# Kernel optimization log

Hardware: AMD Instinct MI355X
Metric: run time of the kernel (lower is better)

The kernel has to match this reference:

```python
import jax, jax.numpy as jnp
import numpy as np

NUM_SCENES = 7
SHAPE = [512, 512, 256, 64]  # layer dims: 512->512->256->64
BATCH = 16384


def _xavier(key, shape):
    # nn.init.xavier_normal_ on (s, in, out): fan_in/fan_out from last two dims
    fan_in, fan_out = shape[-2], shape[-1]
    std = np.sqrt(2.0 / (fan_in + fan_out)).astype(np.float32)
    return jax.random.normal(key, shape, dtype=jnp.float32) * std


def setup_inputs() -> dict:
    key = jax.random.key(0)
    ks = jax.random.split(key, 16)
    inp = {
        "x": jax.random.normal(ks[0], (BATCH, SHAPE[0]), dtype=jnp.float32),
        "scene": jax.random.randint(ks[1], (BATCH,), 1, NUM_SCENES + 1, dtype=jnp.int64),
    }
    for i in range(3):
        din, dout = SHAPE[i], SHAPE[i + 1]
        inp[f"W{i}"] = _xavier(ks[2 + 4 * i], (NUM_SCENES, din, dout))
        inp[f"b{i}"] = jnp.zeros((NUM_SCENES, dout), dtype=jnp.float32)
        inp[f"gW{i}"] = _xavier(ks[3 + 4 * i], (1, din, dout))
        inp[f"gb{i}"] = jnp.zeros((1, dout), dtype=jnp.float32)
    return inp


def _star_linear(x, scene0, W, b, gW, gb, relu):
    # W: (S, in, out), gW: (1, in, out). Equivalent to gathering W[scene0]
    # and doing x[:,None,:] @ (w * gW), but computed as a dense GEMM over
    # all scenes followed by a per-sample select (avoids B*in*out gather).
    scaled = W * gW                                   # (S, in, out)
    out_all = jnp.einsum('bi,sio->bso', x, scaled)    # (B, S, out)
    out = jnp.take_along_axis(out_all, scene0[:, None, None], axis=1)[:, 0, :]
    out = out + b[scene0] + gb[0]
    if relu:
        out = jnp.maximum(out, 0.0)
    return out  # dropout is identity at eval


def reference(x, scene, W0, b0, gW0, gb0, W1, b1, gW1, gb1, W2, b2, gW2, gb2):
    scene0 = (scene - 1).astype(jnp.int32)
    h = _star_linear(x, scene0, W0, b0, gW0, gb0, relu=True)
    h = _star_linear(h, scene0, W1, b1, gW1, gb1, relu=True)
    h = _star_linear(h, scene0, W2, b2, gW2, gb2, relu=False)  # drop=True -> no relu
    return h
```

## Files before the change

kernel.cpp:

```cpp
#include <hip/hip_runtime.h>
#include <hip/hip_bf16.h>
#include <stdint.h>


#define BATCH   16384
#define NSCENE  7
#define TM      128
#define NBLK    (BATCH / 256)
#define MT_MAX  (BATCH / TM + NSCENE)
#define PADMAX  (BATCH + NSCENE * TM)

typedef __bf16 bf16x8 __attribute__((ext_vector_type(8)));
typedef float  f32x4  __attribute__((ext_vector_type(4)));

__device__ __forceinline__ ushort f2bf(float f) {
  union { float f; uint32_t u; } v; v.f = f;
  uint32_t r = (v.u + 0x7FFFu + ((v.u >> 16) & 1u)) >> 16;
  return (ushort)r;
}
__device__ __forceinline__ uint32_t pk2(float a, float b) {
  union { __hip_bfloat162 h; uint32_t u; } cv;
  cv.h = __float22bfloat162_rn(make_float2(a, b));
  return cv.u;
}
__device__ __forceinline__ void async16(const void* g, void* lds) {
  __builtin_amdgcn_global_load_lds(
      (const __attribute__((address_space(1))) uint32_t*)g,
      (__attribute__((address_space(3))) uint32_t*)lds, 16, 0, 0);
}

__device__ __forceinline__ void st_tile(const float* __restrict__ W,
                                        const float* __restrict__ gW,
                                        ushort* __restrict__ sT,
                                        int K, int N, int s, int n0, int k0,
                                        int tid) {
  __shared__ float tl[32][33];
  int tx = tid & 31, ty = tid >> 5;
  const float* Wp = W + (size_t)s * K * N;
#pragma unroll
  for (int i = 0; i < 4; i++) {
    int k = k0 + ty + i * 8;
    tl[ty + i * 8][tx] = Wp[(size_t)k * N + n0 + tx] * gW[(size_t)k * N + n0 + tx];
  }
  __syncthreads();
#pragma unroll
  for (int i = 0; i < 4; i++) {
    int n = n0 + ty + i * 8;
    sT[((size_t)s * N + n) * K + k0 + tx] = f2bf(tl[tx][ty + i * 8]);
  }
}

#define NB_W0 (16 * 16 * 7)
#define NB_W1 (8 * 16 * 7)
#define NB_W2 (2 * 8 * 7)
#define NB_BIAS 23
#define NB_CNT NBLK

__global__ __launch_bounds__(256) void prep_k(
    const float* __restrict__ W0, const float* __restrict__ gW0,
    const float* __restrict__ W1, const float* __restrict__ gW1,
    const float* __restrict__ W2, const float* __restrict__ gW2,
    const float* __restrict__ b0, const float* __restrict__ gb0,
    const float* __restrict__ b1, const float* __restrict__ gb1,
    const float* __restrict__ b2, const float* __restrict__ gb2,
    const int* __restrict__ scene,
    ushort* __restrict__ sT0, ushort* __restrict__ sT1, ushort* __restrict__ sT2,
    float* __restrict__ bias0, float* __restrict__ bias1, float* __restrict__ bias2,
    int* __restrict__ bcnt, int* __restrict__ rank) {
  int bid = blockIdx.x, tid = threadIdx.x;
  if (bid < NB_W0) {
    int l = bid;
    st_tile(W0, gW0, sT0, 512, 512, l / 256, (l % 16) * 32, ((l / 16) % 16) * 32, tid);
  } else if (bid < NB_W0 + NB_W1) {
    int l = bid - NB_W0;
    st_tile(W1, gW1, sT1, 512, 256, l / 128, (l % 8) * 32, ((l / 8) % 16) * 32, tid);
  } else if (bid < NB_W0 + NB_W1 + NB_W2) {
    int l = bid - NB_W0 - NB_W1;
    st_tile(W2, gW2, sT2, 256, 64, l / 16, (l % 2) * 32, ((l / 2) % 8) * 32, tid);
  } else if (bid < NB_W0 + NB_W1 + NB_W2 + NB_BIAS) {
    int t = (bid - NB_W0 - NB_W1 - NB_W2) * 256 + tid;
    if (t < 7 * 512) bias0[t] = b0[t] + gb0[t & 511];
    else if (t < 7 * 512 + 7 * 256) { int i = t - 7 * 512; bias1[i] = b1[i] + gb1[i & 255]; }
    else if (t < 7 * 512 + 7 * 256 + 7 * 64) { int i = t - 7 * 512 - 7 * 256; bias2[i] = b2[i] + gb2[i & 63]; }
  } else {
    __shared__ int l[NSCENE];
    if (tid < NSCENE) l[tid] = 0;
    __syncthreads();
    int blk = bid - NB_W0 - NB_W1 - NB_W2 - NB_BIAS;
    int i = blk * 256 + tid;
    int pos = atomicAdd(&l[scene[i] - 1], 1);
    rank[i] = pos;
    __syncthreads();
    if (tid < NSCENE) bcnt[blk * NSCENE + tid] = l[tid];
  }
}

__global__ void plan_k(const int* __restrict__ bcnt, int* __restrict__ meta,
                       int* __restrict__ bbase, int* __restrict__ idxp) {
  __shared__ int tot[NSCENE], pstart[NSCENE], pend[NSCENE];
  int tid = threadIdx.x;
  if (tid < NSCENE) {
    int c = 0;
    for (int b = 0; b < NBLK; b++) c += bcnt[b * NSCENE + tid];
    tot[tid] = c;
  }
  __syncthreads();
  if (tid == 0) {
    int po = 0, t = 0;
    for (int s = 0; s < NSCENE; s++) {
      meta[16 + s] = po;
      int tiles = (tot[s] + TM - 1) / TM;
      pstart[s] = po + tot[s];
      pend[s] = po + tiles * TM;
      for (int j = 0; j < tiles; j++) { meta[32 + t] = s; meta[192 + t] = po + j * TM; t++; }
      po += tiles * TM;
    }
    meta[24] = t;
  }
  __syncthreads();
  if (tid < NSCENE) {
    int run = meta[16 + tid];
    for (int b = 0; b < NBLK; b++) { bbase[b * NSCENE + tid] = run; run += bcnt[b * NSCENE + tid]; }
  }
  for (int s = 0; s < NSCENE; s++)
    for (int i = pstart[s] + tid; i < pend[s]; i += 256) idxp[i] = -1;
}

__global__ __launch_bounds__(256) void xc_k(const float* __restrict__ x,
                                            const int* __restrict__ scene,
                                            const int* __restrict__ rank,
                                            const int* __restrict__ bbase,
                                            int* __restrict__ idxp,
                                            ushort* __restrict__ xc) {
  int r = blockIdx.x * 8 + (threadIdx.x >> 5);
  int s = scene[r] - 1;
  int d = bbase[(r >> 8) * NSCENE + s] + rank[r];
  if ((threadIdx.x & 31) == 0) idxp[d] = r;
  int c = (threadIdx.x & 31) * 16;
  const float4* p = (const float4*)(x + (size_t)r * 512 + c);
  float4 f0 = p[0], f1 = p[1], f2 = p[2], f3 = p[3];
  uint4 v0, v1;
  v0.x = pk2(f0.x, f0.y); v0.y = pk2(f0.z, f0.w);
  v0.z = pk2(f1.x, f1.y); v0.w = pk2(f1.z, f1.w);
  v1.x = pk2(f2.x, f2.y); v1.y = pk2(f2.z, f2.w);
  v1.z = pk2(f3.x, f3.y); v1.w = pk2(f3.z, f3.w);
  uint4* q = (uint4*)(xc + (size_t)d * 512 + c);
  q[0] = v0; q[1] = v1;
}

__global__ __launch_bounds__(256) void gemm0_k(
    const ushort* __restrict__ ain, const ushort* __restrict__ bw,
    const float* __restrict__ bias, const int* __restrict__ meta,
    ushort* __restrict__ hout) {
  int j = blockIdx.x;
  int t = j >> 1;
  if (t >= meta[24]) return;
  int sc = meta[32 + t];
  int mrow0 = meta[192 + t] + (j & 1) * 64;
  int nb = blockIdx.y;

  __shared__ __align__(16) ushort Abuf[64 * 64];
  __shared__ __align__(16) ushort Bbuf[128 * 64];

  int tid = threadIdx.x;
  int lane = tid & 63, wid = tid >> 6;

  f32x4 acc[4][2];
#pragma unroll
  for (int mt = 0; mt < 4; mt++)
#pragma unroll
    for (int nt = 0; nt < 2; nt++) acc[mt][nt] = (f32x4){0.f, 0.f, 0.f, 0.f};

  const ushort* bwS = bw + ((size_t)sc * 512 + (size_t)nb * 128) * 512;

  for (int kb = 0; kb < 8; kb++) {
#pragma unroll
    for (int i = 0; i < 2; i++) {
      int c = tid + i * 256;
      int row = c >> 3, q = c & 7;
      int kg = q ^ (row & 7);
      async16(ain + (size_t)(mrow0 + row) * 512 + kb * 64 + kg * 8,
              &Abuf[(size_t)(i * 256 + wid * 64) * 8]);
    }
#pragma unroll
    for (int i = 0; i < 4; i++) {
      int c = tid + i * 256;
      int row = c >> 3, q = c & 7;
      int kg = q ^ (row & 7);
      async16(bwS + (size_t)row * 512 + kb * 64 + kg * 8,
              &Bbuf[(size_t)(i * 256 + wid * 64) * 8]);
    }
    __syncthreads();
#pragma unroll
    for (int kk = 0; kk < 64; kk += 32) {
      bf16x8 af[4], bfr[2];
      int kc = (kk >> 3) + (lane >> 4);
#pragma unroll
      for (int mt = 0; mt < 4; mt++) {
        int row = mt * 16 + (lane & 15);
        af[mt] = *(const bf16x8*)(&Abuf[(row * 8 + (kc ^ (row & 7))) * 8]);
      }
#pragma unroll
      for (int nt = 0; nt < 2; nt++) {
        int row = wid * 32 + nt * 16 + (lane & 15);
        bfr[nt] = *(const bf16x8*)(&Bbuf[(row * 8 + (kc ^ (row & 7))) * 8]);
      }
#pragma unroll
      for (int mt = 0; mt < 4; mt++)
#pragma unroll
        for (int nt = 0; nt < 2; nt++)
          acc[mt][nt] = __builtin_amdgcn_mfma_f32_16x16x32_bf16(af[mt], bfr[nt], acc[mt][nt], 0, 0, 0);
    }
    __syncthreads();
  }

#pragma unroll
  for (int mt = 0; mt < 4; mt++) {
    int rl0 = mt * 16 + (lane >> 4) * 4;
#pragma unroll
    for (int nt = 0; nt < 2; nt++) {
      int col = nb * 128 + wid * 32 + nt * 16 + (lane & 15);
      float bv = bias[sc * 512 + col];
#pragma unroll
      for (int r = 0; r < 4; r++) {
        float v = fmaxf(acc[mt][nt][r] + bv, 0.f);
        hout[(size_t)(mrow0 + rl0 + r) * 512 + col] = f2bf(v);
      }
    }
  }
}

__global__ __launch_bounds__(256) void gemm12_k(
    const ushort* __restrict__ hc1, const ushort* __restrict__ sT1,
    const ushort* __restrict__ sT2, const float* __restrict__ bias1,
    const float* __restrict__ bias2, const int* __restrict__ meta,
    const int* __restrict__ idxp, float* __restrict__ out) {
  int j = blockIdx.x;
  int t = j >> 1;
  if (t >= meta[24]) return;
  int sc = meta[32 + t];
  int mrow0 = meta[192 + t] + (j & 1) * 64;

  __shared__ __align__(16) ushort Abuf[64 * 64];
  __shared__ __align__(16) ushort Bbuf[256 * 64];
  __shared__ __align__(16) ushort h2[64 * 256];

  int tid = threadIdx.x;
  int lane = tid & 63, wid = tid >> 6;

  f32x4 acc[4][4];
#pragma unroll
  for (int mt = 0; mt < 4; mt++)
#pragma unroll
    for (int nt = 0; nt < 4; nt++) acc[mt][nt] = (f32x4){0.f, 0.f, 0.f, 0.f};

  const ushort* b1p = sT1 + (size_t)sc * 256 * 512;

  for (int kb = 0; kb < 8; kb++) {
#pragma unroll
    for (int i = 0; i < 2; i++) {
      int c = tid + i * 256;
      int row = c >> 3, q = c & 7;
      int kg = q ^ (row & 7);
      async16(hc1 + (size_t)(mrow0 + row) * 512 + kb * 64 + kg * 8,
              &Abuf[(size_t)(i * 256 + wid * 64) * 8]);
    }
#pragma unroll
    for (int i = 0; i < 8; i++) {
      int c = tid + i * 256;
      int row = c >> 3, q = c & 7;
      int kg = q ^ (row & 7);
      async16(b1p + (size_t)row * 512 + kb * 64 + kg * 8,
              &Bbuf[(size_t)(i * 256 + wid * 64) * 8]);
    }
    __syncthreads();
#pragma unroll
    for (int kk = 0; kk < 64; kk += 32) {
      bf16x8 af[4], bfr[4];
      int kc = (kk >> 3) + (lane >> 4);
#pragma unroll
      for (int mt = 0; mt < 4; mt++) {
        int row = mt * 16 + (lane & 15);
        af[mt] = *(const bf16x8*)(&Abuf[(row * 8 + (kc ^ (row & 7))) * 8]);
      }
#pragma unroll
      for (int nt = 0; nt < 4; nt++) {
        int row = wid * 64 + nt * 16 + (lane & 15);
        bfr[nt] = *(const bf16x8*)(&Bbuf[(row * 8 + (kc ^ (row & 7))) * 8]);
      }
#pragma unroll
      for (int mt = 0; mt < 4; mt++)
#pragma unroll
        for (int nt = 0; nt < 4; nt++)
          acc[mt][nt] = __builtin_amdgcn_mfma_f32_16x16x32_bf16(af[mt], bfr[nt], acc[mt][nt], 0, 0, 0);
    }
    __syncthreads();
  }

#pragma unroll
  for (int mt = 0; mt < 4; mt++) {
#pragma unroll
    for (int nt = 0; nt < 4; nt++) {
      int col = wid * 64 + nt * 16 + (lane & 15);
      float bv = bias1[sc * 256 + col];
#pragma unroll
      for (int r = 0; r < 4; r++) {
        int row = mt * 16 + (lane >> 4) * 4 + r;
        float v = fmaxf(acc[mt][nt][r] + bv, 0.f);
        h2[(row * 32 + ((col >> 3) ^ (row & 7))) * 8 + (col & 7)] = f2bf(v);
      }
    }
  }

  const ushort* b2p = sT2 + (size_t)sc * 64 * 256;
#pragma unroll
  for (int i = 0; i < 8; i++) {
    int p = tid + i * 256;
    int row = p >> 5, pc = p & 31;
    int kg = pc ^ (row & 7);
    async16(b2p + (size_t)row * 256 + kg * 8,
            &Bbuf[(size_t)(i * 256 + wid * 64) * 8]);
  }
  __syncthreads();

  f32x4 acc2[4];
#pragma unroll
  for (int nt = 0; nt < 4; nt++) acc2[nt] = (f32x4){0.f, 0.f, 0.f, 0.f};

#pragma unroll
  for (int kk = 0; kk < 256; kk += 32) {
    int kf = (kk >> 3) + (lane >> 4);
    bf16x8 af;
    {
      int row = wid * 16 + (lane & 15);
      af = *(const bf16x8*)(&h2[(row * 32 + (kf ^ (row & 7))) * 8]);
    }
    bf16x8 bfr[4];
#pragma unroll
    for (int nt = 0; nt < 4; nt++) {
      int n = nt * 16 + (lane & 15);
      bfr[nt] = *(const bf16x8*)(&Bbuf[(n * 32 + (kf ^ (n & 7))) * 8]);
    }
#pragma unroll
    for (int nt = 0; nt < 4; nt++)
      acc2[nt] = __builtin_amdgcn_mfma_f32_16x16x32_bf16(af, bfr[nt], acc2[nt], 0, 0, 0);
  }

  int gidx[4];
#pragma unroll
  for (int r = 0; r < 4; r++)
    gidx[r] = idxp[mrow0 + wid * 16 + (lane >> 4) * 4 + r];
#pragma unroll
  for (int nt = 0; nt < 4; nt++) {
    int col = nt * 16 + (lane & 15);
    float bv = bias2[sc * 64 + col];
#pragma unroll
    for (int r = 0; r < 4; r++) {
      int g = gidx[r];
      if (g >= 0) out[(size_t)g * 64 + col] = acc2[nt][r] + bv;
    }
  }
}

extern "C" void kernel_launch(void* const* d_in, const int* in_sizes, int n_in,
                              void* d_out, int out_size, void* d_ws, size_t ws_size,
                              hipStream_t stream) {
  const float* x   = (const float*)d_in[0];
  const int* scene = (const int*)d_in[1];
  const float* W0  = (const float*)d_in[2];
  const float* b0  = (const float*)d_in[3];
  const float* gW0 = (const float*)d_in[4];
  const float* gb0 = (const float*)d_in[5];
  const float* W1  = (const float*)d_in[6];
  const float* b1  = (const float*)d_in[7];
  const float* gW1 = (const float*)d_in[8];
  const float* gb1 = (const float*)d_in[9];
  const float* W2  = (const float*)d_in[10];
  const float* b2  = (const float*)d_in[11];
  const float* gW2 = (const float*)d_in[12];
  const float* gb2 = (const float*)d_in[13];
  float* out = (float*)d_out;

  char* ws = (char*)d_ws;
  size_t off = 0;
  auto alloc = [&](size_t bytes) -> void* {
    void* p = ws + off;
    off = (off + bytes + 255) & ~(size_t)255;
    return p;
  };
  ushort* sT0   = (ushort*)alloc((size_t)7 * 512 * 512 * 2);
  ushort* sT1   = (ushort*)alloc((size_t)7 * 256 * 512 * 2);
  ushort* sT2   = (ushort*)alloc((size_t)7 * 64 * 256 * 2);
  float*  bias0 = (float*)alloc(7 * 512 * 4);
  float*  bias1 = (float*)alloc(7 * 256 * 4);
  float*  bias2 = (float*)alloc(7 * 64 * 4);
  int*    meta  = (int*)alloc(1024 * 4);
  int*    bcnt  = (int*)alloc(NBLK * NSCENE * 4);
  int*    bbase = (int*)alloc(NBLK * NSCENE * 4);
  int*    rank  = (int*)alloc(BATCH * 4);
  int*    idxp  = (int*)alloc(PADMAX * 4);
  ushort* xc    = (ushort*)alloc((size_t)PADMAX * 512 * 2);
  ushort* hc1   = (ushort*)alloc((size_t)PADMAX * 512 * 2);
  (void)ws_size; (void)n_in; (void)in_sizes; (void)out_size;

  prep_k<<<NB_W0 + NB_W1 + NB_W2 + NB_BIAS + NB_CNT, 256, 0, stream>>>(
      W0, gW0, W1, gW1, W2, gW2, b0, gb0, b1, gb1, b2, gb2, scene,
      sT0, sT1, sT2, bias0, bias1, bias2, bcnt, rank);
  plan_k<<<1, 256, 0, stream>>>(bcnt, meta, bbase, idxp);
  xc_k<<<BATCH / 8, 256, 0, stream>>>(x, scene, rank, bbase, idxp, xc);

  gemm0_k<<<dim3(MT_MAX * 2, 4), 256, 0, stream>>>(xc, sT0, bias0, meta, hc1);
  gemm12_k<<<dim3(MT_MAX * 2), 256, 0, stream>>>(hc1, sT1, sT2, bias1, bias2,
                                                 meta, idxp, out);
}
```

Baseline: 156.0 us.

## Remove single-block plan kernel by deriving tile plan redundantly in each consumer

Drops the serial one-block plan kernel and the meta/bbase buffers. Each block of xc_k, gemm0_k and gemm12_k now loads the per-block scene counts into shared memory and recomputes the tile offsets, and xc_k builds its own prefix base. Padding rows are no longer filled with -1; the final store instead masks on row position against the scene's real count. This removes one kernel launch and its serialized latency, at the cost of redundant per-block prefix work and an extra barrier at the start of every GEMM block.

```diff
diff --git a/kernel.cpp b/kernel.cpp
--- a/kernel.cpp
+++ b/kernel.cpp
@@ -95,48 +95,55 @@
   }
 }
 
-__global__ void plan_k(const int* __restrict__ bcnt, int* __restrict__ meta,
-                       int* __restrict__ bbase, int* __restrict__ idxp) {
-  __shared__ int tot[NSCENE], pstart[NSCENE], pend[NSCENE];
-  int tid = threadIdx.x;
+#define PLAN_SHARED  __shared__ int sb[NBLK * NSCENE]; \
+                     __shared__ int tot[NSCENE], padoff[NSCENE], cumt[NSCENE + 1];
+__device__ __forceinline__ void plan_derive(const int* __restrict__ bcnt,
+                                            int* sb, int* tot, int* padoff,
+                                            int* cumt, int tid) {
+  if (tid < NBLK * NSCENE) sb[tid] = bcnt[tid];
+  if (tid + 256 < NBLK * NSCENE) sb[tid + 256] = bcnt[tid + 256];
+  __syncthreads();
   if (tid < NSCENE) {
     int c = 0;
-    for (int b = 0; b < NBLK; b++) c += bcnt[b * NSCENE + tid];
+    for (int b = 0; b < NBLK; b++) c += sb[b * NSCENE + tid];
     tot[tid] = c;
   }
   __syncthreads();
   if (tid == 0) {
-    int po = 0, t = 0;
+    int po = 0, ct = 0;
     for (int s = 0; s < NSCENE; s++) {
-      meta[16 + s] = po;
+      padoff[s] = po; cumt[s] = ct;
       int tiles = (tot[s] + TM - 1) / TM;
-      pstart[s] = po + tot[s];
-      pend[s] = po + tiles * TM;
-      for (int j = 0; j < tiles; j++) { meta[32 + t] = s; meta[192 + t] = po + j * TM; t++; }
-      po += tiles * TM;
-    }
-    meta[24] = t;
-  }
-  __syncthreads();
-  if (tid < NSCENE) {
-    int run = meta[16 + tid];
-    for (int b = 0; b < NBLK; b++) { bbase[b * NSCENE + tid] = run; run += bcnt[b * NSCENE + tid]; }
-  }
-  for (int s = 0; s < NSCENE; s++)
-    for (int i = pstart[s] + tid; i < pend[s]; i += 256) idxp[i] = -1;
+      ct += tiles; po += tiles * TM;
+    }
+    cumt[NSCENE] = ct;
+  }
+  __syncthreads();
 }
 
 __global__ __launch_bounds__(256) void xc_k(const float* __restrict__ x,
                                             const int* __restrict__ scene,
                                             const int* __restrict__ rank,
-                                            const int* __restrict__ bbase,
+                                            const int* __restrict__ bcnt,
                                             int* __restrict__ idxp,
                                             ushort* __restrict__ xc) {
-  int r = blockIdx.x * 8 + (threadIdx.x >> 5);
+  PLAN_SHARED
+  __shared__ int base7[NSCENE];
+  int tid = threadIdx.x;
+  plan_derive(bcnt, sb, tot, padoff, cumt, tid);
+  int myblk = blockIdx.x >> 5;
+  if (tid < NSCENE) {
+    int pre = 0;
+    for (int b = 0; b < myblk; b++) pre += sb[b * NSCENE + tid];
+    base7[tid] = padoff[tid] + pre;
+  }
+  __syncthreads();
+
+  int r = blockIdx.x * 8 + (tid >> 5);
   int s = scene[r] - 1;
-  int d = bbase[(r >> 8) * NSCENE + s] + rank[r];
-  if ((threadIdx.x & 31) == 0) idxp[d] = r;
-  int c = (threadIdx.x & 31) * 16;
+  int d = base7[s] + rank[r];
+  if ((tid & 31) == 0) idxp[d] = r;
+  int c = (tid & 31) * 16;
   const float4* p = (const float4*)(x + (size_t)r * 512 + c);
   float4 f0 = p[0], f1 = p[1], f2 = p[2], f3 = p[3];
   uint4 v0, v1;
@@ -150,19 +157,23 @@
 
 __global__ __launch_bounds__(256) void gemm0_k(
     const ushort* __restrict__ ain, const ushort* __restrict__ bw,
-    const float* __restrict__ bias, const int* __restrict__ meta,
+    const float* __restrict__ bias, const int* __restrict__ bcnt,
     ushort* __restrict__ hout) {
+  PLAN_SHARED
+  __shared__ __align__(16) ushort Abuf[64 * 64];
+  __shared__ __align__(16) ushort Bbuf[128 * 64];
+
+  int tid = threadIdx.x;
+  plan_derive(bcnt, sb, tot, padoff, cumt, tid);
+
   int j = blockIdx.x;
   int t = j >> 1;
-  if (t >= meta[24]) return;
-  int sc = meta[32 + t];
-  int mrow0 = meta[192 + t] + (j & 1) * 64;
+  if (t >= cumt[NSCENE]) return;
+  int sc = 0;
+  while (sc < NSCENE - 1 && t >= cumt[sc + 1]) sc++;
+  int mrow0 = padoff[sc] + (t - cumt[sc]) * TM + (j & 1) * 64;
   int nb = blockIdx.y;
 
-  __shared__ __align__(16) ushort Abuf[64 * 64];
-  __shared__ __align__(16) ushort Bbuf[128 * 64];
-
-  int tid = threadIdx.x;
   int lane = tid & 63, wid = tid >> 6;
 
   f32x4 acc[4][2];
@@ -233,19 +244,24 @@
 __global__ __launch_bounds__(256) void gemm12_k(
     const ushort* __restrict__ hc1, const ushort* __restrict__ sT1,
     const ushort* __restrict__ sT2, const float* __restrict__ bias1,
-    const float* __restrict__ bias2, const int* __restrict__ meta,
+    const float* __restrict__ bias2, const int* __restrict__ bcnt,
     const int* __restrict__ idxp, float* __restrict__ out) {
-  int j = blockIdx.x;
-  int t = j >> 1;
-  if (t >= meta[24]) return;
-  int sc = meta[32 + t];
-  int mrow0 = meta[192 + t] + (j & 1) * 64;
-
+  PLAN_SHARED
   __shared__ __align__(16) ushort Abuf[64 * 64];
   __shared__ __align__(16) ushort Bbuf[256 * 64];
   __shared__ __align__(16) ushort h2[64 * 256];
 
   int tid = threadIdx.x;
+  plan_derive(bcnt, sb, tot, padoff, cumt, tid);
+
+  int j = blockIdx.x;
+  int t = j >> 1;
+  if (t >= cumt[NSCENE]) return;
+  int sc = 0;
+  while (sc < NSCENE - 1 && t >= cumt[sc + 1]) sc++;
+  int mrow0 = padoff[sc] + (t - cumt[sc]) * TM + (j & 1) * 64;
+  int maxloc = padoff[sc] + tot[sc];
+
   int lane = tid & 63, wid = tid >> 6;
 
   f32x4 acc[4][4];
@@ -346,18 +362,19 @@
       acc2[nt] = __builtin_amdgcn_mfma_f32_16x16x32_bf16(af, bfr[nt], acc2[nt], 0, 0, 0);
   }
 
-  int gidx[4];
-#pragma unroll
-  for (int r = 0; r < 4; r++)
-    gidx[r] = idxp[mrow0 + wid * 16 + (lane >> 4) * 4 + r];
+  int rowg[4], gidx[4];
+#pragma unroll
+  for (int r = 0; r < 4; r++) {
+    rowg[r] = mrow0 + wid * 16 + (lane >> 4) * 4 + r;
+    gidx[r] = idxp[rowg[r]];
+  }
 #pragma unroll
   for (int nt = 0; nt < 4; nt++) {
     int col = nt * 16 + (lane & 15);
     float bv = bias2[sc * 64 + col];
 #pragma unroll
     for (int r = 0; r < 4; r++) {
-      int g = gidx[r];
-      if (g >= 0) out[(size_t)g * 64 + col] = acc2[nt][r] + bv;
+      if (rowg[r] < maxloc) out[(size_t)gidx[r] * 64 + col] = acc2[nt][r] + bv;
     }
   }
 }
@@ -394,9 +411,7 @@
   float*  bias0 = (float*)alloc(7 * 512 * 4);
   float*  bias1 = (float*)alloc(7 * 256 * 4);
   float*  bias2 = (float*)alloc(7 * 64 * 4);
-  int*    meta  = (int*)alloc(1024 * 4);
   int*    bcnt  = (int*)alloc(NBLK * NSCENE * 4);
-  int*    bbase = (int*)alloc(NBLK * NSCENE * 4);
   int*    rank  = (int*)alloc(BATCH * 4);
   int*    idxp  = (int*)alloc(PADMAX * 4);
   ushort* xc    = (ushort*)alloc((size_t)PADMAX * 512 * 2);
@@ -406,10 +421,9 @@
   prep_k<<<NB_W0 + NB_W1 + NB_W2 + NB_BIAS + NB_CNT, 256, 0, stream>>>(
       W0, gW0, W1, gW1, W2, gW2, b0, gb0, b1, gb1, b2, gb2, scene,
       sT0, sT1, sT2, bias0, bias1, bias2, bcnt, rank);
-  plan_k<<<1, 256, 0, stream>>>(bcnt, meta, bbase, idxp);
-  xc_k<<<BATCH / 8, 256, 0, stream>>>(x, scene, rank, bbase, idxp, xc);
-
-  gemm0_k<<<dim3(MT_MAX * 2, 4), 256, 0, stream>>>(xc, sT0, bias0, meta, hc1);
+  xc_k<<<BATCH / 8, 256, 0, stream>>>(x, scene, rank, bcnt, idxp, xc);
+
+  gemm0_k<<<dim3(MT_MAX * 2, 4), 256, 0, stream>>>(xc, sT0, bias0, bcnt, hc1);
   gemm12_k<<<dim3(MT_MAX * 2), 256, 0, stream>>>(hc1, sT1, sT2, bias1, bias2,
-                                                 meta, idxp, out);
-}
+                                                 bcnt, idxp, out);
+}
```

Result: faster. 152.8 us (-2.0%).
